# Kernel tuning notes

Hardware: AMD Instinct MI355X
Metric: run time of the kernel (lower is better)

The kernel has to match this reference:

```python
import jax, jax.numpy as jnp
import numpy as np

B, C, H, W = 4, 256, 128, 256
NUM_CODES = 256  # codebook rows; dim_code == C


def setup_inputs() -> dict:
    key = jax.random.key(0)
    k_feat, k_code = jax.random.split(key)
    feature = jax.random.normal(k_feat, (B, C, H, W), dtype=jnp.float32)
    codebook = jax.random.normal(k_code, (NUM_CODES, C), dtype=jnp.float32)
    return {"feature": feature, "codebook": codebook}


def reference(feature, codebook):
    # Faithful to ComminPub.sender core:
    #   weights = (feature_expand * codebooks).sum(dim=2) / (codebooks*codebooks).sum(dim=2)
    # expressed as a contraction over C instead of materializing [B,N,C,H,W].
    code_norm = jnp.sum(codebook * codebook, axis=1)          # [N]
    weights = jnp.einsum('bchw,nc->bnhw', feature, codebook)   # [B,N,H,W]
    weights = weights / code_norm[None, :, None, None]
    # fc_after_rbdc reconstruction: einsum('b n h w, n c -> b c h w', weights, codebook)
    recon = jnp.einsum('bnhw,nc->bchw', weights, codebook)     # [B,C,H,W]
    return recon
```

## Files before the change

kernel.cpp:

```cpp
#include <hip/hip_runtime.h>
#include <hip/hip_bf16.h>
#include <cstdint>

#define CDIM   256
#define NCODES 256
#define HWB    32768
#define BATCH  4
#define BN     128
#define NTILES 4
#define TPB    512

typedef __bf16 bf16x8 __attribute__((ext_vector_type(8)));
typedef float  f32x4  __attribute__((ext_vector_type(4)));

__global__ __launch_bounds__(256) void prep_kernel(const float* __restrict__ cb,
                                                   __bf16* __restrict__ Mb) {
    __shared__ float s[NCODES];
    const int i = blockIdx.x;
    const int j = threadIdx.x;

    const float* row = cb + (size_t)j * CDIM;
    float nrm = 0.f;
#pragma unroll 8
    for (int c = 0; c < CDIM; c += 4) {
        f32x4 v = *(const f32x4*)(row + c);
        nrm += v[0] * v[0] + v[1] * v[1] + v[2] * v[2] + v[3] * v[3];
    }
    s[j] = cb[(size_t)j * CDIM + i] / nrm;
    __syncthreads();

    float acc = 0.f;
#pragma unroll 16
    for (int n = 0; n < NCODES; ++n)
        acc += s[n] * cb[(size_t)n * CDIM + j];
    Mb[(size_t)i * CDIM + j] = (__bf16)acc;
}

__global__ __launch_bounds__(TPB, 2) void recon_kernel(
    const float* __restrict__ feat, const __bf16* __restrict__ Mb,
    float* __restrict__ out) {
    __shared__ __align__(16) __bf16 Blds[2][BN * 32];

    const int tid  = threadIdx.x;
    const int lane = tid & 63;
    const int w    = tid >> 6;
    const int quad = lane >> 4;
    const int l16  = lane & 15;
    const int r0   = w * 32;

    const __bf16* mb = Mb + (size_t)(r0 + l16) * CDIM + quad * 8;
    bf16x8 mreg[2][8];
#pragma unroll
    for (int mt = 0; mt < 2; ++mt)
#pragma unroll
        for (int kc = 0; kc < 8; ++kc)
            mreg[mt][kc] = *(const bf16x8*)(mb + (size_t)mt * 16 * CDIM + kc * 32);

    const int spx   = lane + (w & 1) * 64;
    const int sk0   = (w >> 1) * 8;
    const int swoff = spx * 32 + (((w >> 1) ^ ((spx >> 1) & 3)) * 8);
    const int rdoff = (quad ^ ((l16 >> 1) & 3)) * 8;

    const int b        = blockIdx.x >> 6;
    const int px_base0 = (blockIdx.x & 63) * (BN * NTILES);

    const float* fB = feat + (size_t)b * CDIM * HWB;
    float*       oB = out  + (size_t)b * CDIM * HWB;

    for (int ti = 0; ti < NTILES; ++ti) {
        const int p0 = px_base0 + ti * BN;
        const float* fs = fB + p0 + spx + (size_t)sk0 * HWB;

        float fv[3][8];
#pragma unroll
        for (int c = 0; c < 3; ++c)
#pragma unroll
            for (int j = 0; j < 8; ++j)
                fv[c][j] = fs[(size_t)(c * 32 + j) * HWB];

        f32x4 acc[2][8];
#pragma unroll
        for (int mt = 0; mt < 2; ++mt)
#pragma unroll
            for (int nt = 0; nt < 8; ++nt)
                acc[mt][nt] = (f32x4){0.f, 0.f, 0.f, 0.f};

#pragma unroll
        for (int i = 0; i < 8; ++i) {
            bf16x8 pk;
#pragma unroll
            for (int j = 0; j < 8; ++j) pk[j] = (__bf16)fv[i % 3][j];
            if (i < 5) {
#pragma unroll
                for (int j = 0; j < 8; ++j)
                    fv[i % 3][j] = fs[(size_t)((i + 3) * 32 + j) * HWB];
            }
            *(bf16x8*)(&Blds[i & 1][0] + swoff) = pk;
            asm volatile("s_waitcnt lgkmcnt(0)\n\ts_barrier" ::: "memory");
#pragma unroll
            for (int nt = 0; nt < 8; ++nt) {
                bf16x8 bfr = *(const bf16x8*)(
                    &Blds[i & 1][0] + (nt * 16 + l16) * 32 + rdoff);
                acc[0][nt] = __builtin_amdgcn_mfma_f32_16x16x32_bf16(
                    mreg[0][i], bfr, acc[0][nt], 0, 0, 0);
                acc[1][nt] = __builtin_amdgcn_mfma_f32_16x16x32_bf16(
                    mreg[1][i], bfr, acc[1][nt], 0, 0, 0);
            }
        }

        float* ob = oB + p0 + l16;
#pragma unroll
        for (int mt = 0; mt < 2; ++mt)
#pragma unroll
            for (int r = 0; r < 4; ++r) {
                float* orow = ob + (size_t)(r0 + mt * 16 + quad * 4 + r) * HWB;
#pragma unroll
                for (int nt = 0; nt < 8; ++nt)
                    orow[nt * 16] = acc[mt][nt][r];
            }
    }
}

extern "C" void kernel_launch(void* const* d_in, const int* in_sizes, int n_in,
                              void* d_out, int out_size, void* d_ws, size_t ws_size,
                              hipStream_t stream) {
    const float* feat = (const float*)d_in[0];
    const float* cb   = (const float*)d_in[1];
    float* out = (float*)d_out;

    __bf16* Mb = (__bf16*)d_ws;

    prep_kernel<<<NCODES, 256, 0, stream>>>(cb, Mb);

    recon_kernel<<<256, TPB, 0, stream>>>(feat, Mb, out);
}
```

Baseline: 257.8 us.

## Swap MFMA operand roles, vectorize feature loads and output stores, one tile per block

The recon kernel now places pixels on the MFMA A operand and the projection matrix on B. This lets each lane write four consecutive output pixels as one 16-byte store, and lets features be loaded as float4 along the pixel dimension instead of scalar strided loads. The prep kernel writes the matrix in a k-packed layout so the B fragments load contiguously, and it computes two rows per block. The LDS tile gains a padded row stride. The grid grows to one 128-pixel tile per block, which drops the per-block loop and reloads the matrix fragments in every block.

```diff
diff --git a/kernel.cpp b/kernel.cpp
--- a/kernel.cpp
+++ b/kernel.cpp
@@ -7,17 +7,21 @@
 #define HWB    32768
 #define BATCH  4
 #define BN     128
-#define NTILES 4
 #define TPB    512
+#define LROW   36
 
-typedef __bf16 bf16x8 __attribute__((ext_vector_type(8)));
-typedef float  f32x4  __attribute__((ext_vector_type(4)));
+typedef __bf16  bf16x8 __attribute__((ext_vector_type(8)));
+typedef __bf16  bf16x2 __attribute__((ext_vector_type(2)));
+typedef float   f32x4  __attribute__((ext_vector_type(4)));
+typedef float   f32x2  __attribute__((ext_vector_type(2)));
+typedef uint32_t u32x2 __attribute__((ext_vector_type(2)));
+typedef uint32_t u32x4 __attribute__((ext_vector_type(4)));
 
 __global__ __launch_bounds__(256) void prep_kernel(const float* __restrict__ cb,
-                                                   __bf16* __restrict__ Mb) {
-    __shared__ float s[NCODES];
-    const int i = blockIdx.x;
-    const int j = threadIdx.x;
+                                                   __bf16* __restrict__ Mpk) {
+    __shared__ f32x2 s2[NCODES];
+    const int i0 = blockIdx.x * 2;
+    const int j  = threadIdx.x;
 
     const float* row = cb + (size_t)j * CDIM;
     float nrm = 0.f;
@@ -26,99 +30,102 @@
         f32x4 v = *(const f32x4*)(row + c);
         nrm += v[0] * v[0] + v[1] * v[1] + v[2] * v[2] + v[3] * v[3];
     }
-    s[j] = cb[(size_t)j * CDIM + i] / nrm;
+    const float inv = 1.0f / nrm;
+    s2[j] = (f32x2){row[i0] * inv, row[i0 + 1] * inv};
     __syncthreads();
 
-    float acc = 0.f;
+    f32x2 acc = {0.f, 0.f};
 #pragma unroll 16
-    for (int n = 0; n < NCODES; ++n)
-        acc += s[n] * cb[(size_t)n * CDIM + j];
-    Mb[(size_t)i * CDIM + j] = (__bf16)acc;
+    for (int n = 0; n < NCODES; ++n) {
+        const float cv = cb[(size_t)n * CDIM + j];
+        const f32x2 sv = s2[n];
+        acc[0] += sv[0] * cv;
+        acc[1] += sv[1] * cv;
+    }
+    const int base = ((j >> 3) * 256) * 8 + (j & 7);
+    Mpk[base + (size_t)(i0    ) * 8] = (__bf16)acc[0];
+    Mpk[base + (size_t)(i0 + 1) * 8] = (__bf16)acc[1];
 }
 
 __global__ __launch_bounds__(TPB, 2) void recon_kernel(
-    const float* __restrict__ feat, const __bf16* __restrict__ Mb,
+    const float* __restrict__ feat, const __bf16* __restrict__ Mpk,
     float* __restrict__ out) {
-    __shared__ __align__(16) __bf16 Blds[2][BN * 32];
+    __shared__ __align__(16) __bf16 Blds[2][BN * LROW];
 
     const int tid  = threadIdx.x;
     const int lane = tid & 63;
     const int w    = tid >> 6;
     const int quad = lane >> 4;
     const int l16  = lane & 15;
-    const int r0   = w * 32;
+    const int c0   = w * 32;
 
-    const __bf16* mb = Mb + (size_t)(r0 + l16) * CDIM + quad * 8;
     bf16x8 mreg[2][8];
 #pragma unroll
-    for (int mt = 0; mt < 2; ++mt)
+    for (int ct = 0; ct < 2; ++ct)
 #pragma unroll
         for (int kc = 0; kc < 8; ++kc)
-            mreg[mt][kc] = *(const bf16x8*)(mb + (size_t)mt * 16 * CDIM + kc * 32);
+            mreg[ct][kc] = *(const bf16x8*)(
+                Mpk + (size_t)((kc * 4 + quad) * 256 + c0 + ct * 16 + l16) * 8);
 
-    const int spx   = lane + (w & 1) * 64;
-    const int sk0   = (w >> 1) * 8;
-    const int swoff = spx * 32 + (((w >> 1) ^ ((spx >> 1) & 3)) * 8);
-    const int rdoff = (quad ^ ((l16 >> 1) & 3)) * 8;
+    const int b  = blockIdx.x >> 8;
+    const int p0 = (blockIdx.x & 255) * BN;
 
-    const int b        = blockIdx.x >> 6;
-    const int px_base0 = (blockIdx.x & 63) * (BN * NTILES);
+    const int px4 = tid & 31;
+    const int kp  = tid >> 5;
+    const float* f0 = feat + (size_t)b * CDIM * HWB + p0 + px4 * 4;
 
-    const float* fB = feat + (size_t)b * CDIM * HWB;
-    float*       oB = out  + (size_t)b * CDIM * HWB;
+    f32x4 acc[8][2];
+#pragma unroll
+    for (int mt = 0; mt < 8; ++mt)
+#pragma unroll
+        for (int ct = 0; ct < 2; ++ct)
+            acc[mt][ct] = (f32x4){0.f, 0.f, 0.f, 0.f};
 
-    for (int ti = 0; ti < NTILES; ++ti) {
-        const int p0 = px_base0 + ti * BN;
-        const float* fs = fB + p0 + spx + (size_t)sk0 * HWB;
+    f32x4 fva[2], fvb[2];
+#pragma unroll
+    for (int s = 0; s < 2; ++s) {
+        fva[s] = *(const f32x4*)(f0 + (size_t)(s * 32 + 2 * kp) * HWB);
+        fvb[s] = *(const f32x4*)(f0 + (size_t)(s * 32 + 2 * kp + 1) * HWB);
+    }
 
-        float fv[3][8];
-#pragma unroll
-        for (int c = 0; c < 3; ++c)
-#pragma unroll
-            for (int j = 0; j < 8; ++j)
-                fv[c][j] = fs[(size_t)(c * 32 + j) * HWB];
-
-        f32x4 acc[2][8];
-#pragma unroll
-        for (int mt = 0; mt < 2; ++mt)
-#pragma unroll
-            for (int nt = 0; nt < 8; ++nt)
-                acc[mt][nt] = (f32x4){0.f, 0.f, 0.f, 0.f};
+    const int rbase = l16 * 18 + quad * 4;
 
 #pragma unroll
-        for (int i = 0; i < 8; ++i) {
-            bf16x8 pk;
+    for (int i = 0; i < 8; ++i) {
+        const int sl = i & 1;
+        __bf16* wb = &Blds[i & 1][0] + (px4 * 4) * LROW + 2 * kp;
 #pragma unroll
-            for (int j = 0; j < 8; ++j) pk[j] = (__bf16)fv[i % 3][j];
-            if (i < 5) {
+        for (int e = 0; e < 4; ++e) {
+            bf16x2 p;
+            p[0] = (__bf16)fva[sl][e];
+            p[1] = (__bf16)fvb[sl][e];
+            *(bf16x2*)(wb + (size_t)e * LROW) = p;
+        }
+        if (i < 6) {
+            fva[sl] = *(const f32x4*)(f0 + (size_t)((i + 2) * 32 + 2 * kp) * HWB);
+            fvb[sl] = *(const f32x4*)(f0 + (size_t)((i + 2) * 32 + 2 * kp + 1) * HWB);
+        }
+        asm volatile("s_waitcnt lgkmcnt(0)\n\ts_barrier" ::: "memory");
+        const uint32_t* lr = (const uint32_t*)(&Blds[i & 1][0]);
 #pragma unroll
-                for (int j = 0; j < 8; ++j)
-                    fv[i % 3][j] = fs[(size_t)((i + 3) * 32 + j) * HWB];
-            }
-            *(bf16x8*)(&Blds[i & 1][0] + swoff) = pk;
-            asm volatile("s_waitcnt lgkmcnt(0)\n\ts_barrier" ::: "memory");
+        for (int mt = 0; mt < 8; ++mt) {
+            u32x2 lo = *(const u32x2*)(lr + rbase + mt * 288);
+            u32x2 hi = *(const u32x2*)(lr + rbase + mt * 288 + 2);
+            bf16x8 af = __builtin_bit_cast(bf16x8, (u32x4){lo[0], lo[1], hi[0], hi[1]});
+            acc[mt][0] = __builtin_amdgcn_mfma_f32_16x16x32_bf16(
+                af, mreg[0][i], acc[mt][0], 0, 0, 0);
+            acc[mt][1] = __builtin_amdgcn_mfma_f32_16x16x32_bf16(
+                af, mreg[1][i], acc[mt][1], 0, 0, 0);
+        }
+    }
+
+    float* ob = out + (size_t)b * CDIM * HWB + p0 + quad * 4;
 #pragma unroll
-            for (int nt = 0; nt < 8; ++nt) {
-                bf16x8 bfr = *(const bf16x8*)(
-                    &Blds[i & 1][0] + (nt * 16 + l16) * 32 + rdoff);
-                acc[0][nt] = __builtin_amdgcn_mfma_f32_16x16x32_bf16(
-                    mreg[0][i], bfr, acc[0][nt], 0, 0, 0);
-                acc[1][nt] = __builtin_amdgcn_mfma_f32_16x16x32_bf16(
-                    mreg[1][i], bfr, acc[1][nt], 0, 0, 0);
-            }
-        }
-
-        float* ob = oB + p0 + l16;
+    for (int mt = 0; mt < 8; ++mt)
 #pragma unroll
-        for (int mt = 0; mt < 2; ++mt)
-#pragma unroll
-            for (int r = 0; r < 4; ++r) {
-                float* orow = ob + (size_t)(r0 + mt * 16 + quad * 4 + r) * HWB;
-#pragma unroll
-                for (int nt = 0; nt < 8; ++nt)
-                    orow[nt * 16] = acc[mt][nt][r];
-            }
-    }
+        for (int ct = 0; ct < 2; ++ct)
+            *(f32x4*)(ob + (size_t)(c0 + ct * 16 + l16) * HWB + mt * 16) =
+                acc[mt][ct];
 }
 
 extern "C" void kernel_launch(void* const* d_in, const int* in_sizes, int n_in,
@@ -128,9 +135,10 @@
     const float* cb   = (const float*)d_in[1];
     float* out = (float*)d_out;
 
-    __bf16* Mb = (__bf16*)d_ws;
+    __bf16* Mpk = (__bf16*)d_ws;
 
-    prep_kernel<<<NCODES, 256, 0, stream>>>(cb, Mb);
+    prep_kernel<<<NCODES / 2, 256, 0, stream>>>(cb, Mpk);
 
-    recon_kernel<<<256, TPB, 0, stream>>>(feat, Mb, out);
+    const int nblocks = BATCH * (HWB / BN);
+    recon_kernel<<<nblocks, TPB, 0, stream>>>(feat, Mpk, out);
 }
```

Result: faster. 248.4 us (-3.6%).
